# Optimization experiments

Measured on AMD Instinct MI355X. Metric: run time of the kernel, lower is better.

## Reference

```python
import jax, jax.numpy as jnp
import numpy as np

SENTINEL = 24635
NUM_ENTITIES = 24636
EMB_DIM = 128


def setup_inputs() -> dict:
    key = jax.random.key(0)
    ks = jax.random.split(key, 6)
    B, L = 4096, 50
    return {
        "encoded_context_embs": jax.random.normal(ks[0], (B, 1024), jnp.float32),
        "ent_embs": jax.random.normal(ks[1], (NUM_ENTITIES, EMB_DIM), jnp.float32) * 0.02,
        "W1": jax.random.normal(ks[2], (768, 1024), jnp.float32) * 0.02,
        "W2": jax.random.normal(ks[3], (512, 768), jnp.float32) * 0.02,
        "W3": jax.random.normal(ks[4], (128, 512), jnp.float32) * 0.02,
        "ent_list": jax.random.randint(ks[5], (B, L), 0, NUM_ENTITIES, jnp.int64),
    }


def reference(encoded_context_embs, ent_embs, W1, W2, W3, ent_list):
    # --- ragged gather + masked mean with sentinel early-exit ---
    # valid[b, l] == 1 iff no sentinel appeared at positions <= l (prefix-AND)
    not_sent = (ent_list != SENTINEL).astype(ent_embs.dtype)   # [B, L]
    valid = jnp.cumprod(not_sent, axis=1)                      # [B, L]
    gathered = ent_embs[ent_list]                              # [B, L, D]
    cnt = valid.sum(axis=1)                                    # [B]
    summed = jnp.einsum("bl,bld->bd", valid, gathered)        # [B, D]
    mean = summed / jnp.maximum(cnt, 1.0)[:, None]
    # sentinel at position 0 -> fall back to the sentinel embedding
    user_embs = jnp.where((cnt == 0)[:, None], ent_embs[SENTINEL][None, :], mean)

    # --- MLP on pooled context: 1024 -> 768 -> 512 -> 128 ---
    x = jax.nn.relu(encoded_context_embs @ W1.T)
    x = jax.nn.relu(x @ W2.T)
    q = x @ W3.T                                               # [B, 128]

    # --- cross attention: query=q, key=value=user_embs ---
    scale = 1.0 / jnp.sqrt(jnp.asarray(q.shape[-1], q.dtype))
    scores = (q @ user_embs.T) * scale                         # [B, B]
    weights = jax.nn.softmax(scores, axis=-1)
    return weights @ user_embs                                 # [B, 128]
```

## Files before the change

kernel.cpp:

```cpp
#include <hip/hip_runtime.h>
#include <hip/hip_bf16.h>

#define SENTINEL 24635

typedef unsigned char f8_t;
using bf16x8  = __attribute__((ext_vector_type(8))) __bf16;
using bf16x2  = __attribute__((ext_vector_type(2))) __bf16;
using floatx4 = __attribute__((ext_vector_type(4))) float;

__device__ inline int pack4_fp8(float4 a, float s) {
  int w = __builtin_amdgcn_cvt_pk_fp8_f32(a.x * s, a.y * s, 0, false);
  return __builtin_amdgcn_cvt_pk_fp8_f32(a.z * s, a.w * s, w, true);
}

__device__ inline void store_fp8x8(f8_t* d, float4 a, float4 b, float s) {
  int2 v; v.x = pack4_fp8(a, s); v.y = pack4_fp8(b, s);
  *(int2*)d = v;
}

__device__ inline void gll16(const void* g, void* l) {
  __builtin_amdgcn_global_load_lds(
      (const __attribute__((address_space(1))) unsigned int*)g,
      (__attribute__((address_space(3))) unsigned int*)l, 16, 0, 0);
}

__device__ inline void pool_body(const float* __restrict__ ent,
                                 const int* __restrict__ ent_list,
                                 __bf16* __restrict__ user_n, int b) {
  const int lane = threadIdx.x & 63;
  int myidx = (lane < 50) ? ent_list[b * 50 + lane] : 0;
  unsigned long long m = __ballot(lane < 50 && myidx == SENTINEL);
  const int cnt = (m == 0) ? 50 : (int)__builtin_ctzll(m);

  float sx = 0.f, sy = 0.f;
  for (int l0 = 0; l0 < 50; l0 += 10) {
    if (l0 >= cnt) break;
    float2 e[10];
#pragma unroll
    for (int j = 0; j < 10; ++j) {
      int idx = __shfl(myidx, l0 + j);
      e[j] = *(const float2*)(ent + (size_t)idx * 128 + lane * 2);
    }
#pragma unroll
    for (int j = 0; j < 10; ++j) {
      if (l0 + j < cnt) { sx += e[j].x; sy += e[j].y; }
    }
  }
  float vx, vy;
  if (cnt == 0) {
    float2 e = *(const float2*)(ent + (size_t)SENTINEL * 128 + lane * 2);
    vx = e.x; vy = e.y;
  } else {
    float inv = 1.f / (float)cnt;
    vx = sx * inv; vy = sy * inv;
  }
  bf16x2 o; o[0] = (__bf16)vx; o[1] = (__bf16)vy;
  *(bf16x2*)(user_n + (size_t)b * 128 + lane * 2) = o;
}

__global__ __launch_bounds__(256) void prep_kernel(
    const float* __restrict__ s0, f8_t* __restrict__ d0,
    const float* __restrict__ s1, f8_t* __restrict__ d1) {
  int g = blockIdx.x * 256 + threadIdx.x;
  const float* s; f8_t* d; int i; float sc;
  if (g < 524288)      { s = s0; d = d0; i = g;          sc = 1.f;  }
  else                 { s = s1; d = d1; i = g - 524288; sc = 16.f; }
  i *= 8;
  float4 a = *(const float4*)(s + i);
  float4 b = *(const float4*)(s + i + 4);
  store_fp8x8(d + i, a, b, sc);
}

template <int WR, int WC, int MT, int NT, int RELU, bool OUT_BF16, int NS>
__device__ inline void gemm_body_f8(const f8_t* __restrict__ A,
                                    const f8_t* __restrict__ W,
                                    void* __restrict__ Cout,
                                    int M, int N, int K, int bn0, int bm0,
                                    char* lds) {
  constexpr int BM = WR * MT * 16;
  constexpr int BN = WC * NT * 16;
  auto As = (f8_t (*)[BM][32])lds;
  auto Bs = (f8_t (*)[BN][32])(lds + (size_t)NS * BM * 32);
  const int tid  = threadIdx.x;
  const int w    = tid >> 6;
  const int lane = tid & 63;
  const int quad = lane >> 4;
  const int l16  = lane & 15;
  const int wr   = w / WC;
  const int wc   = w % WC;
  const int lrow = lane >> 1;
  const int lcol = (lane & 1) * 16;

  floatx4 acc[MT][NT];
#pragma unroll
  for (int mt = 0; mt < MT; ++mt)
#pragma unroll
    for (int nt = 0; nt < NT; ++nt) acc[mt][nt] = (floatx4){0.f, 0.f, 0.f, 0.f};

  constexpr int nAc = NS * (BM / 32);
  constexpr int nBc = NS * (BN / 32);
  for (int k0 = 0; k0 < K; k0 += NS * 32) {
    __syncthreads();
#pragma unroll
    for (int c = w; c < nAc; c += 4) {
      int s = c / (BM / 32);
      int r = (c % (BM / 32)) * 32;
      gll16(A + (size_t)(bm0 + r + lrow) * K + k0 + s * 32 + lcol, &As[s][r][0]);
    }
#pragma unroll
    for (int c = w; c < nBc; c += 4) {
      int s = c / (BN / 32);
      int r = (c % (BN / 32)) * 32;
      gll16(W + (size_t)(bn0 + r + lrow) * K + k0 + s * 32 + lcol, &Bs[s][r][0]);
    }
    __syncthreads();
#pragma unroll
    for (int s = 0; s < NS; ++s) {
      long af[MT], bfr[NT];
#pragma unroll
      for (int mt = 0; mt < MT; ++mt)
        af[mt] = *(const long*)&As[s][wr * (MT * 16) + mt * 16 + l16][quad * 8];
#pragma unroll
      for (int nt = 0; nt < NT; ++nt)
        bfr[nt] = *(const long*)&Bs[s][wc * (NT * 16) + nt * 16 + l16][quad * 8];
#pragma unroll
      for (int mt = 0; mt < MT; ++mt)
#pragma unroll
        for (int nt = 0; nt < NT; ++nt)
          acc[mt][nt] = __builtin_amdgcn_mfma_f32_16x16x32_fp8_fp8(
              af[mt], bfr[nt], acc[mt][nt], 0, 0, 0);
    }
  }

  const float osc = 0.0625f;
#pragma unroll
  for (int mt = 0; mt < MT; ++mt) {
    const int row0 = bm0 + wr * (MT * 16) + mt * 16 + quad * 4;
#pragma unroll
    for (int nt = 0; nt < NT; ++nt) {
      const int col = bn0 + wc * (NT * 16) + nt * 16 + l16;
#pragma unroll
      for (int r = 0; r < 4; ++r) {
        float v = acc[mt][nt][r] * osc;
        if (RELU) v = fmaxf(v, 0.f);
        if (OUT_BF16) {
          ((__bf16*)Cout)[(size_t)(row0 + r) * N + col] = (__bf16)v;
        } else {
          int p = __builtin_amdgcn_cvt_pk_fp8_f32(v, v, 0, false);
          ((f8_t*)Cout)[(size_t)(row0 + r) * N + col] = (f8_t)(p & 0xff);
        }
      }
    }
  }
}

template <int WR, int WC, int MT, int NT, int RELU, bool OUT_BF16, int NS>
__global__ __launch_bounds__(256) void gemm_f8(const f8_t* __restrict__ A,
                                               const f8_t* __restrict__ W,
                                               void* __restrict__ C,
                                               int M, int N, int K) {
  __shared__ char lds[(size_t)NS * ((WR * MT * 16) + (WC * NT * 16)) * 32];
  gemm_body_f8<WR, WC, MT, NT, RELU, OUT_BF16, NS>(
      A, W, C, M, N, K, blockIdx.x * (WC * NT * 16), blockIdx.y * (WR * MT * 16),
      lds);
}

__global__ __launch_bounds__(256) void gemm1_pool(const f8_t* __restrict__ A,
                                                  const f8_t* __restrict__ W,
                                                  f8_t* __restrict__ C,
                                                  const float* __restrict__ ent,
                                                  const int* __restrict__ ent_list,
                                                  __bf16* __restrict__ user_n,
                                                  const float* __restrict__ s2,
                                                  f8_t* __restrict__ d2,
                                                  const float* __restrict__ s3,
                                                  f8_t* __restrict__ d3) {
  __shared__ char lds[20480];
  const int bx = blockIdx.x;
  if (bx < 512) {
    gemm_body_f8<2, 2, 2, 3, 1, false, 4>(A, W, C, 4096, 768, 1024,
                                          (bx % 8) * 96, (bx / 8) * 64, lds);
    return;
  }
  if (bx < 1536) {
    pool_body(ent, ent_list, user_n, (bx - 512) * 4 + (threadIdx.x >> 6));
    return;
  }
  int g = (bx - 1536) * 256 + threadIdx.x;
  const float* s; f8_t* d; int i;
  if (g < 49152) { s = s2; d = d2; i = g; }
  else           { s = s3; d = d3; i = g - 49152; }
  i *= 8;
  float4 a = *(const float4*)(s + i);
  float4 b = *(const float4*)(s + i + 4);
  store_fp8x8(d + i, a, b, 16.f);
}

__global__ __launch_bounds__(256) void gemm2_tr(const f8_t* __restrict__ A,
                                                const f8_t* __restrict__ W,
                                                f8_t* __restrict__ C,
                                                const __bf16* __restrict__ un,
                                                __bf16* __restrict__ ut) {
  __shared__ char lds[16384];
  const int bx = blockIdx.x;
  if (bx < 512) {
    gemm_body_f8<2, 2, 2, 2, 1, false, 4>(A, W, C, 4096, 512, 768,
                                          (bx % 8) * 64, (bx / 8) * 64, lds);
    return;
  }
  const int idx = bx - 512;
  const int r0 = (idx & 63) * 64;
  const int c0 = (idx >> 6) * 64;
  auto T = (__bf16 (*)[72])lds;
  const int tid = threadIdx.x;
#pragma unroll
  for (int p = 0; p < 2; ++p) {
    int r = (tid >> 3) + p * 32;
    int c = (tid & 7) * 8;
    *(bf16x8*)&T[r][c] = *(const bf16x8*)(un + (size_t)(r0 + r) * 128 + c0 + c);
  }
  __syncthreads();
#pragma unroll
  for (int p = 0; p < 2; ++p) {
    int c = (tid >> 3) + p * 32;
    int r = (tid & 7) * 8;
    bf16x8 v;
#pragma unroll
    for (int j = 0; j < 8; ++j) v[j] = T[r + j][c];
    *(bf16x8*)(ut + (size_t)(c0 + c) * 4096 + r0 + r) = v;
  }
}

__global__ __launch_bounds__(256) void flash_attn(const __bf16* __restrict__ Q,
                                                  const __bf16* __restrict__ Un_g,
                                                  const __bf16* __restrict__ Ut_g,
                                                  __bf16* __restrict__ O_part,
                                                  float* __restrict__ lp) {
  __shared__ __bf16 Un[64][136];
  __shared__ __bf16 Ut[128][72];
  __shared__ __bf16 Ps[4][32][72];
  const int tid  = threadIdx.x;
  const int w    = tid >> 6;
  const int lane = tid & 63;
  const int quad = lane >> 4;
  const int l16  = lane & 15;
  const int qrow0 = blockIdx.x * 128;
  const int split = blockIdx.y;
  const float scale = 0.08838834764831845f;

  bf16x8 aq[2][4];
#pragma unroll
  for (int mt = 0; mt < 2; ++mt)
#pragma unroll
    for (int c = 0; c < 4; ++c)
      aq[mt][c] = *(const bf16x8*)(Q + (size_t)(qrow0 + w * 32 + mt * 16 + l16) * 128 +
                                   c * 32 + quad * 8);

  floatx4 o[2][8];
#pragma unroll
  for (int mt = 0; mt < 2; ++mt)
#pragma unroll
    for (int t = 0; t < 8; ++t) o[mt][t] = (floatx4){0.f, 0.f, 0.f, 0.f};
  float lsum[2][4] = {{0.f, 0.f, 0.f, 0.f}, {0.f, 0.f, 0.f, 0.f}};

  const int sr = tid >> 4, sc = (tid & 15) * 8;
  const int td = tid >> 3, tk = (tid & 7) * 8;
  bf16x8 un_r[4], ut_r[4];

#define LD_CHUNK(key0)                                                         \
  do {                                                                         \
    _Pragma("unroll")                                                          \
    for (int p = 0; p < 4; ++p)                                                \
      un_r[p] = *(const bf16x8*)(Un_g + (size_t)((key0) + sr + p * 16) * 128 + sc); \
    _Pragma("unroll")                                                          \
    for (int p = 0; p < 4; ++p)                                                \
      ut_r[p] = *(const bf16x8*)(Ut_g + (size_t)(td + p * 32) * 4096 + (key0) + tk); \
  } while (0)

#define ST_CHUNK()                                                             \
  do {                                                                         \
    _Pragma("unroll")                                                          \
    for (int p = 0; p < 4; ++p) *(bf16x8*)&Un[sr + p * 16][sc] = un_r[p];      \
    _Pragma("unroll")                                                          \
    for (int p = 0; p < 4; ++p) *(bf16x8*)&Ut[td + p * 32][tk] = ut_r[p];      \
  } while (0)

  LD_CHUNK(split * 256);
  ST_CHUNK();
  __syncthreads();

  for (int chunk = 0; chunk < 4; ++chunk) {
    if (chunk < 3) LD_CHUNK(split * 256 + (chunk + 1) * 64);

#pragma unroll
    for (int t = 0; t < 4; ++t) {
      bf16x8 bk[4];
#pragma unroll
      for (int c = 0; c < 4; ++c)
        bk[c] = *(const bf16x8*)&Un[t * 16 + l16][c * 32 + quad * 8];
      floatx4 s0 = (floatx4){0.f, 0.f, 0.f, 0.f};
      floatx4 s1 = (floatx4){0.f, 0.f, 0.f, 0.f};
      __builtin_amdgcn_s_setprio(1);
#pragma unroll
      for (int c = 0; c < 4; ++c) {
        s0 = __builtin_amdgcn_mfma_f32_16x16x32_bf16(aq[0][c], bk[c], s0, 0, 0, 0);
        s1 = __builtin_amdgcn_mfma_f32_16x16x32_bf16(aq[1][c], bk[c], s1, 0, 0, 0);
      }
      __builtin_amdgcn_s_setprio(0);
#pragma unroll
      for (int r = 0; r < 4; ++r) {
        float p0 = __expf(s0[r] * scale);
        float p1 = __expf(s1[r] * scale);
        lsum[0][r] += p0;
        lsum[1][r] += p1;
        Ps[w][quad * 4 + r][t * 16 + l16] = (__bf16)p0;
        Ps[w][16 + quad * 4 + r][t * 16 + l16] = (__bf16)p1;
      }
    }

#pragma unroll
    for (int c2 = 0; c2 < 2; ++c2) {
      bf16x8 ap0 = *(const bf16x8*)&Ps[w][l16][c2 * 32 + quad * 8];
      bf16x8 ap1 = *(const bf16x8*)&Ps[w][16 + l16][c2 * 32 + quad * 8];
      __builtin_amdgcn_s_setprio(1);
#pragma unroll
      for (int dt = 0; dt < 8; ++dt) {
        bf16x8 bv = *(const bf16x8*)&Ut[dt * 16 + l16][c2 * 32 + quad * 8];
        o[0][dt] = __builtin_amdgcn_mfma_f32_16x16x32_bf16(ap0, bv, o[0][dt], 0, 0, 0);
        o[1][dt] = __builtin_amdgcn_mfma_f32_16x16x32_bf16(ap1, bv, o[1][dt], 0, 0, 0);
      }
      __builtin_amdgcn_s_setprio(0);
    }

    if (chunk < 3) {
      __syncthreads();
      ST_CHUNK();
      __syncthreads();
    }
  }
#undef LD_CHUNK
#undef ST_CHUNK

#pragma unroll
  for (int mt = 0; mt < 2; ++mt)
#pragma unroll
    for (int r = 0; r < 4; ++r) {
      float v = lsum[mt][r];
      v += __shfl_xor(v, 1);
      v += __shfl_xor(v, 2);
      v += __shfl_xor(v, 4);
      v += __shfl_xor(v, 8);
      lsum[mt][r] = v;
    }

  __bf16* Ob = O_part + (size_t)split * 524288;
#pragma unroll
  for (int mt = 0; mt < 2; ++mt) {
    const int row0 = qrow0 + w * 32 + mt * 16 + quad * 4;
#pragma unroll
    for (int dt = 0; dt < 8; ++dt) {
#pragma unroll
      for (int r = 0; r < 4; ++r) {
        Ob[(size_t)(row0 + r) * 128 + dt * 16 + l16] = (__bf16)o[mt][dt][r];
      }
    }
    if (l16 == 0) {
#pragma unroll
      for (int r = 0; r < 4; ++r) lp[(size_t)split * 4096 + row0 + r] = lsum[mt][r];
    }
  }
}

__global__ __launch_bounds__(256) void combine_kernel(const __bf16* __restrict__ Op,
                                                      const float* __restrict__ lp,
                                                      float* __restrict__ out) {
  const int i = (blockIdx.x * 256 + threadIdx.x) * 8;
  const int row = i >> 7;
  float num[8] = {0.f, 0.f, 0.f, 0.f, 0.f, 0.f, 0.f, 0.f};
  float den = 0.f;
#pragma unroll
  for (int s = 0; s < 16; ++s) {
    bf16x8 v = *(const bf16x8*)(Op + (size_t)s * 524288 + i);
#pragma unroll
    for (int j = 0; j < 8; ++j) num[j] += (float)v[j];
    den += lp[(size_t)s * 4096 + row];
  }
  float inv = 1.f / den;
  float4 r0 = {num[0] * inv, num[1] * inv, num[2] * inv, num[3] * inv};
  float4 r1 = {num[4] * inv, num[5] * inv, num[6] * inv, num[7] * inv};
  *(float4*)(out + i) = r0;
  *(float4*)(out + i + 4) = r1;
}

extern "C" void kernel_launch(void* const* d_in, const int* in_sizes, int n_in,
                              void* d_out, int out_size, void* d_ws, size_t ws_size,
                              hipStream_t stream) {
  (void)in_sizes; (void)n_in; (void)out_size; (void)ws_size;
  const float* ctx      = (const float*)d_in[0];
  const float* ent_embs = (const float*)d_in[1];
  const float* W1       = (const float*)d_in[2];
  const float* W2       = (const float*)d_in[3];
  const float* W3       = (const float*)d_in[4];
  const int*   ent_list = (const int*)d_in[5];
  float* out = (float*)d_out;

  char* base = (char*)d_ws;
  __bf16* user_n = (__bf16*)(base);
  __bf16* user_t = (__bf16*)(base + (1ull << 20));
  __bf16* qb     = (__bf16*)(base + (2ull << 20));
  float*  lp     = (float*)(base + (3ull << 20));
  f8_t*   ctxb   = (f8_t*)(base + (4ull << 20));
  f8_t*   W1b    = (f8_t*)(base + (8ull << 20));
  f8_t*   W2b    = (f8_t*)(base + 9175040ull);
  f8_t*   W3b    = (f8_t*)(base + 9568256ull);
  f8_t*   x1b    = (f8_t*)(base + (10ull << 20));
  f8_t*   x2b    = (f8_t*)(base + (13ull << 20));
  __bf16* O_part = (__bf16*)(base + (15ull << 20));

  prep_kernel<<<2432, 256, 0, stream>>>(ctx, ctxb, W1, W1b);
  gemm1_pool<<<1760, 256, 0, stream>>>(ctxb, W1b, x1b, ent_embs, ent_list,
                                       user_n, W2, W2b, W3, W3b);
  gemm2_tr<<<640, 256, 0, stream>>>(x1b, W2b, x2b, user_n, user_t);
  gemm_f8<2, 2, 1, 1, 0, true, 4><<<dim3(4, 128), 256, 0, stream>>>(
      x2b, W3b, qb, 4096, 128, 512);
  flash_attn<<<dim3(32, 16), 256, 0, stream>>>(qb, user_n, user_t, O_part, lp);
  combine_kernel<<<256, 256, 0, stream>>>(O_part, lp, out);
}
```

Measured before the change: 141.1 us.

## Fuse final W3 projection GEMM into flash attention prologue

Removes the separate fp8 GEMM kernel that produced the bf16 query matrix and instead computes each block's 128 query rows inside flash_attn with fp8 MFMAs, staging them through shared memory that is later reused for key tiles. This saves one kernel launch and the global round trip of the query tensor. In exchange, the query projection is recomputed redundantly by each of the 16 key splits per query block, and the fused kernel uses more registers and shared memory.

```diff
diff --git a/kernel.cpp b/kernel.cpp
--- a/kernel.cpp
+++ b/kernel.cpp
@@ -154,17 +154,6 @@
   }
 }
 
-template <int WR, int WC, int MT, int NT, int RELU, bool OUT_BF16, int NS>
-__global__ __launch_bounds__(256) void gemm_f8(const f8_t* __restrict__ A,
-                                               const f8_t* __restrict__ W,
-                                               void* __restrict__ C,
-                                               int M, int N, int K) {
-  __shared__ char lds[(size_t)NS * ((WR * MT * 16) + (WC * NT * 16)) * 32];
-  gemm_body_f8<WR, WC, MT, NT, RELU, OUT_BF16, NS>(
-      A, W, C, M, N, K, blockIdx.x * (WC * NT * 16), blockIdx.y * (WR * MT * 16),
-      lds);
-}
-
 __global__ __launch_bounds__(256) void gemm1_pool(const f8_t* __restrict__ A,
                                                   const f8_t* __restrict__ W,
                                                   f8_t* __restrict__ C,
@@ -231,14 +220,17 @@
   }
 }
 
-__global__ __launch_bounds__(256) void flash_attn(const __bf16* __restrict__ Q,
+__global__ __launch_bounds__(256) void flash_attn(const f8_t* __restrict__ X2,
+                                                  const f8_t* __restrict__ W3,
                                                   const __bf16* __restrict__ Un_g,
                                                   const __bf16* __restrict__ Ut_g,
                                                   __bf16* __restrict__ O_part,
                                                   float* __restrict__ lp) {
-  __shared__ __bf16 Un[64][136];
-  __shared__ __bf16 Ut[128][72];
-  __shared__ __bf16 Ps[4][32][72];
+  __shared__ char smem[54272];
+  auto Un = (__bf16 (*)[136])smem;
+  auto Ut = (__bf16 (*)[72])(smem + 17408);
+  auto Ps = (__bf16 (*)[32][72])(smem + 35840);
+  auto Qlds = (__bf16 (*)[136])smem;
   const int tid  = threadIdx.x;
   const int w    = tid >> 6;
   const int lane = tid & 63;
@@ -247,21 +239,6 @@
   const int qrow0 = blockIdx.x * 128;
   const int split = blockIdx.y;
   const float scale = 0.08838834764831845f;
-
-  bf16x8 aq[2][4];
-#pragma unroll
-  for (int mt = 0; mt < 2; ++mt)
-#pragma unroll
-    for (int c = 0; c < 4; ++c)
-      aq[mt][c] = *(const bf16x8*)(Q + (size_t)(qrow0 + w * 32 + mt * 16 + l16) * 128 +
-                                   c * 32 + quad * 8);
-
-  floatx4 o[2][8];
-#pragma unroll
-  for (int mt = 0; mt < 2; ++mt)
-#pragma unroll
-    for (int t = 0; t < 8; ++t) o[mt][t] = (floatx4){0.f, 0.f, 0.f, 0.f};
-  float lsum[2][4] = {{0.f, 0.f, 0.f, 0.f}, {0.f, 0.f, 0.f, 0.f}};
 
   const int sr = tid >> 4, sc = (tid & 15) * 8;
   const int td = tid >> 3, tk = (tid & 7) * 8;
@@ -286,6 +263,52 @@
   } while (0)
 
   LD_CHUNK(split * 256);
+
+  {
+    floatx4 qa[2][8];
+#pragma unroll
+    for (int mt = 0; mt < 2; ++mt)
+#pragma unroll
+      for (int nt = 0; nt < 8; ++nt) qa[mt][nt] = (floatx4){0.f, 0.f, 0.f, 0.f};
+    const f8_t* xr0 = X2 + (size_t)(qrow0 + w * 32 + l16) * 512;
+    const f8_t* xr1 = X2 + (size_t)(qrow0 + w * 32 + 16 + l16) * 512;
+    const f8_t* wb  = W3 + (size_t)l16 * 512;
+#pragma unroll
+    for (int ks = 0; ks < 16; ++ks) {
+      long a0 = *(const long*)(xr0 + ks * 32 + quad * 8);
+      long a1 = *(const long*)(xr1 + ks * 32 + quad * 8);
+#pragma unroll
+      for (int nt = 0; nt < 8; ++nt) {
+        long bf = *(const long*)(wb + (size_t)nt * 16 * 512 + ks * 32 + quad * 8);
+        qa[0][nt] = __builtin_amdgcn_mfma_f32_16x16x32_fp8_fp8(a0, bf, qa[0][nt], 0, 0, 0);
+        qa[1][nt] = __builtin_amdgcn_mfma_f32_16x16x32_fp8_fp8(a1, bf, qa[1][nt], 0, 0, 0);
+      }
+    }
+#pragma unroll
+    for (int mt = 0; mt < 2; ++mt)
+#pragma unroll
+      for (int nt = 0; nt < 8; ++nt)
+#pragma unroll
+        for (int r = 0; r < 4; ++r)
+          Qlds[w * 32 + mt * 16 + quad * 4 + r][nt * 16 + l16] =
+              (__bf16)(qa[mt][nt][r] * 0.0625f);
+  }
+
+  bf16x8 aq[2][4];
+#pragma unroll
+  for (int mt = 0; mt < 2; ++mt)
+#pragma unroll
+    for (int c = 0; c < 4; ++c)
+      aq[mt][c] = *(const bf16x8*)&Qlds[w * 32 + mt * 16 + l16][c * 32 + quad * 8];
+
+  floatx4 o[2][8];
+#pragma unroll
+  for (int mt = 0; mt < 2; ++mt)
+#pragma unroll
+    for (int t = 0; t < 8; ++t) o[mt][t] = (floatx4){0.f, 0.f, 0.f, 0.f};
+  float lsum[2][4] = {{0.f, 0.f, 0.f, 0.f}, {0.f, 0.f, 0.f, 0.f}};
+
+  __syncthreads();
   ST_CHUNK();
   __syncthreads();
 
@@ -407,7 +430,6 @@
   char* base = (char*)d_ws;
   __bf16* user_n = (__bf16*)(base);
   __bf16* user_t = (__bf16*)(base + (1ull << 20));
-  __bf16* qb     = (__bf16*)(base + (2ull << 20));
   float*  lp     = (float*)(base + (3ull << 20));
   f8_t*   ctxb   = (f8_t*)(base + (4ull << 20));
   f8_t*   W1b    = (f8_t*)(base + (8ull << 20));
@@ -421,8 +443,7 @@
   gemm1_pool<<<1760, 256, 0, stream>>>(ctxb, W1b, x1b, ent_embs, ent_list,
                                        user_n, W2, W2b, W3, W3b);
   gemm2_tr<<<640, 256, 0, stream>>>(x1b, W2b, x2b, user_n, user_t);
-  gemm_f8<2, 2, 1, 1, 0, true, 4><<<dim3(4, 128), 256, 0, stream>>>(
-      x2b, W3b, qb, 4096, 128, 512);
-  flash_attn<<<dim3(32, 16), 256, 0, stream>>>(qb, user_n, user_t, O_part, lp);
+  flash_attn<<<dim3(32, 16), 256, 0, stream>>>(x2b, W3b, user_n, user_t,
+                                               O_part, lp);
   combine_kernel<<<256, 256, 0, stream>>>(O_part, lp, out);
 }
```

Measured after the change: 179.7 us. 1.27x slower.
